# Performance work log

Measured on AMD Instinct MI355X. Metric: run time of the kernel, lower is better.

Reference implementation:

```python
import jax, jax.numpy as jnp
import numpy as np

B = 16
N = [20000, 5000, 1250, 313, 79]          # node counts per pooling level (fine -> coarse)
E = [120000, 30000, 7500, 1878, 474]      # ~6 edges per node (triangle mesh)
FILTERS = [3, 32, 32, 64, 64, 64]
K = 6
Z = 64
COND = 2
N_LAYERS = 4


def setup_inputs():
    ks = iter(jax.random.split(jax.random.key(0), 64))
    inp = {}
    inp["x"] = jax.random.normal(next(ks), (B * N[0], FILTERS[0]), jnp.float32)
    inp["label"] = jax.random.normal(next(ks), (B, COND), jnp.float32)
    for i in range(5):
        inp[f"edges{i}"] = jax.random.randint(next(ks), (2, E[i]), 0, N[i])
    for i in range(4):
        inp[f"ds_idx{i}"] = jax.random.randint(next(ks), (N[i + 1],), 0, N[i])
        inp[f"us_idx{i}"] = jax.random.randint(next(ks), (N[i], 3), 0, N[i + 1])
        inp[f"us_w{i}"] = jax.random.uniform(next(ks), (N[i], 3), jnp.float32)
    for i in range(4):
        inp[f"enc_w{i}"] = 0.1 * jax.random.normal(next(ks), (K, FILTERS[i], FILTERS[i + 1]), jnp.float32)
        inp[f"enc_b{i}"] = 0.1 * jax.random.normal(next(ks), (FILTERS[i + 1],), jnp.float32)
    for i in range(5):
        inp[f"dec_w{i}"] = 0.1 * jax.random.normal(next(ks), (K, FILTERS[-i - 1], FILTERS[-i - 2]), jnp.float32)
    for i in range(4):
        inp[f"dec_b{i}"] = 0.1 * jax.random.normal(next(ks), (FILTERS[-i - 2],), jnp.float32)
    lat_in = N[4] * FILTERS[-1]
    inp["enc_mu_w"] = 0.1 * jax.random.normal(next(ks), (lat_in, Z), jnp.float32)
    inp["enc_mu_b"] = jnp.zeros((Z,), jnp.float32)
    inp["enc_lv_w"] = 0.1 * jax.random.normal(next(ks), (lat_in, Z), jnp.float32)
    inp["enc_lv_b"] = jnp.zeros((Z,), jnp.float32)
    inp["dec_lin_w"] = 0.1 * jax.random.normal(next(ks), (Z + COND, lat_in), jnp.float32)
    inp["dec_lin_b"] = jnp.zeros((lat_in,), jnp.float32)
    return inp


def _sym_norm(edges, n):
    # ChebConv_Coma.norm: norm = D^-1/2[row] * w * D^-1/2[col], unit weights
    row, col = edges[0], edges[1]
    deg = jnp.zeros((n,), jnp.float32).at[row].add(1.0)
    dinv = jnp.where(deg > 0, deg ** -0.5, 0.0)
    return dinv[row] * dinv[col]


def _cheb(x, edges, norm, W, b):
    # Chebyshev recursion: Tx_0=x, Tx_1=L~x, Tx_k=2 L~ Tx_{k-1} - Tx_{k-2}
    src, tgt = edges[0], edges[1]

    def prop(h):  # h: [B, Nn, F] -> scatter-sum of norm-weighted source features
        return jnp.zeros_like(h).at[:, tgt].add(h[:, src] * norm[None, :, None])

    Tx0 = x
    out = jnp.einsum('bnf,fg->bng', Tx0, W[0])
    Tx1 = prop(x)
    out = out + jnp.einsum('bnf,fg->bng', Tx1, W[1])
    for k in range(2, W.shape[0]):
        Tx2 = 2.0 * prop(Tx1) - Tx0
        out = out + jnp.einsum('bnf,fg->bng', Tx2, W[k])
        Tx0, Tx1 = Tx1, Tx2
    return out if b is None else out + b


def _forward(x, label, us_ws, enc_ws, enc_bs, dec_ws, dec_bs,
             enc_mu_w, enc_mu_b, enc_lv_w, enc_lv_b, dec_lin_w, dec_lin_b,
             edges, norms, ds_idx, us_idx):
    h = x.reshape(B, N[0], FILTERS[0])
    # encoder
    for i in range(N_LAYERS):
        h = jax.nn.relu(_cheb(h, edges[i], norms[i], enc_ws[i], enc_bs[i]))
        h = h[:, ds_idx[i]]  # binary downsample matrix == row gather
    h = h.reshape(B, N[4] * FILTERS[-1])
    mu = h @ enc_mu_w + enc_mu_b
    logvar = h @ enc_lv_w + enc_lv_b
    # reparameterize (fixed eps for determinism)
    eps = jax.random.normal(jax.random.key(42), mu.shape, mu.dtype)
    z = mu + eps * jnp.exp(0.5 * logvar)
    # decoder
    h = jnp.concatenate([z, label], axis=1)
    h = jax.nn.relu(h @ dec_lin_w + dec_lin_b).reshape(B, N[4], FILTERS[-1])
    for i in range(N_LAYERS):
        lvl = N_LAYERS - 1 - i
        # barycentric upsample: 3 nonzeros per output row
        h = jnp.einsum('rk,brkf->brf', us_ws[lvl], h[:, us_idx[lvl]])
        h = jax.nn.relu(_cheb(h, edges[lvl], norms[lvl], dec_ws[i], dec_bs[i]))
    # faithful quirk of the original: final conv uses A_edge_index[-1] (coarsest graph edges)
    h = _cheb(h, edges[-1], norms[-1], dec_ws[4], None)
    return h.reshape(-1, FILTERS[0]), mu, logvar


def reference(x, label,
              edges0, edges1, edges2, edges3, edges4,
              ds_idx0, ds_idx1, ds_idx2, ds_idx3,
              us_idx0, us_idx1, us_idx2, us_idx3,
              us_w0, us_w1, us_w2, us_w3,
              enc_w0, enc_w1, enc_w2, enc_w3,
              enc_b0, enc_b1, enc_b2, enc_b3,
              dec_w0, dec_w1, dec_w2, dec_w3, dec_w4,
              dec_b0, dec_b1, dec_b2, dec_b3,
              enc_mu_w, enc_mu_b, enc_lv_w, enc_lv_b, dec_lin_w, dec_lin_b):
    edges = [edges0, edges1, edges2, edges3, edges4]
    norms = [_sym_norm(edges[i], N[i]) for i in range(5)]
    return _forward(x, label,
                    [us_w0, us_w1, us_w2, us_w3],
                    [enc_w0, enc_w1, enc_w2, enc_w3],
                    [enc_b0, enc_b1, enc_b2, enc_b3],
                    [dec_w0, dec_w1, dec_w2, dec_w3, dec_w4],
                    [dec_b0, dec_b1, dec_b2, dec_b3],
                    enc_mu_w, enc_mu_b, enc_lv_w, enc_lv_b, dec_lin_w, dec_lin_b,
                    edges, norms,
                    [ds_idx0, ds_idx1, ds_idx2, ds_idx3],
                    [us_idx0, us_idx1, us_idx2, us_idx3])
```

## Files before the change

### kernel.cpp

```cpp
#include <hip/hip_runtime.h>
#include <cstdint>
#include <cstddef>

#define WG 256
#define NB 16



__global__ void k_zero_i(int* __restrict__ p, int n) {
  int i = blockIdx.x * WG + threadIdx.x;
  if (i < n) p[i] = 0;
}

__global__ void k_hist(const int* __restrict__ edges, int E,
                       int* __restrict__ dsrc, int* __restrict__ dtgt) {
  int e = blockIdx.x * WG + threadIdx.x;
  if (e >= E) return;
  atomicAdd(&dsrc[edges[e]], 1);
  atomicAdd(&dtgt[edges[E + e]], 1);
}

__global__ void k_scan(const int* __restrict__ deg, int N,
                       int* __restrict__ rowptr, int* __restrict__ cursor) {
  __shared__ int s[WG];
  int t = threadIdx.x;
  int chunk = (N + WG - 1) / WG;
  int a = t * chunk;
  int b = min(N, a + chunk);
  int sum = 0;
  for (int i = a; i < b; i++) sum += deg[i];
  s[t] = sum;
  __syncthreads();
  for (int off = 1; off < WG; off <<= 1) {
    int v = (t >= off) ? s[t - off] : 0;
    __syncthreads();
    s[t] += v;
    __syncthreads();
  }
  int run = (t == 0) ? 0 : s[t - 1];
  for (int i = a; i < b; i++) {
    rowptr[i] = run;
    cursor[i] = run;
    run += deg[i];
  }
  if (t == 0) rowptr[N] = s[WG - 1];
}

__global__ void k_fill(const int* __restrict__ edges, int E,
                       const int* __restrict__ dsrc, int* __restrict__ cursor,
                       int* __restrict__ csrc, float* __restrict__ csw) {
  int e = blockIdx.x * WG + threadIdx.x;
  if (e >= E) return;
  int s = edges[e], t = edges[E + e];
  float da = (float)dsrc[s], db = (float)dsrc[t];
  float wa = (da > 0.f) ? (1.0f / sqrtf(da)) : 0.f;
  float wb = (db > 0.f) ? (1.0f / sqrtf(db)) : 0.f;
  int pos = atomicAdd(&cursor[t], 1);
  csrc[pos] = s;
  csw[pos] = wa * wb;
}

__global__ void k_tr_x(const float* __restrict__ x, float* __restrict__ out) {
  int i = blockIdx.x * WG + threadIdx.x;
  if (i >= NB * 20000 * 3) return;
  int f = i % 3;
  int b = (i / 3) % NB;
  int n = i / 48;
  out[i] = x[((size_t)b * 20000 + n) * 3 + f];
}


static __device__ __forceinline__ float erfinv_f(float x) {
  float w = -log1pf(-x * x);
  float p;
  if (w < 5.0f) {
    w -= 2.5f;
    p = 2.81022636e-08f;
    p = fmaf(p, w, 3.43273939e-07f);
    p = fmaf(p, w, -3.5233877e-06f);
    p = fmaf(p, w, -4.39150654e-06f);
    p = fmaf(p, w, 0.00021858087f);
    p = fmaf(p, w, -0.00125372503f);
    p = fmaf(p, w, -0.00417768164f);
    p = fmaf(p, w, 0.246640727f);
    p = fmaf(p, w, 1.50140941f);
  } else {
    w = sqrtf(w) - 3.0f;
    p = -0.000200214257f;
    p = fmaf(p, w, 0.000100950558f);
    p = fmaf(p, w, 0.00134934322f);
    p = fmaf(p, w, -0.00367342844f);
    p = fmaf(p, w, 0.00573950773f);
    p = fmaf(p, w, -0.0076224613f);
    p = fmaf(p, w, 0.00943887047f);
    p = fmaf(p, w, 1.00167406f);
    p = fmaf(p, w, 2.83297682f);
  }
  return p * x;
}

static __device__ __forceinline__ float bits_to_normal(unsigned b) {
  float f = __uint_as_float((b >> 9) | 0x3f800000u) - 1.0f;
  const float lo = -0.99999994f;
  float u = f * (1.0f - lo) + lo;
  u = fmaxf(u, lo);
  return 1.41421356f * erfinv_f(u);
}

__global__ void k_eps(float* __restrict__ eps) {
  int i = blockIdx.x * WG + threadIdx.x;
  if (i >= 1024) return;
  unsigned x0 = 0u, x1 = (unsigned)i;
  unsigned ks[3] = {0u, 42u, 0u ^ 42u ^ 0x1BD11BDAu};
  x0 += ks[0];
  x1 += ks[1];
  const int R[2][4] = {{13, 15, 26, 6}, {17, 29, 16, 24}};
#pragma unroll
  for (int it = 0; it < 5; it++) {
#pragma unroll
    for (int j = 0; j < 4; j++) {
      x0 += x1;
      int r = R[it & 1][j];
      x1 = (x1 << r) | (x1 >> (32 - r));
      x1 ^= x0;
    }
    x0 += ks[(it + 1) % 3];
    x1 += ks[(it + 2) % 3] + (unsigned)(it + 1);
  }
  eps[i] = bits_to_normal(x0 ^ x1);
}


template <int F>
__global__ __launch_bounds__(WG) void k_propw(const float* __restrict__ in,
                                              float* __restrict__ out,
                                              const float* __restrict__ sub, float scale,
                                              const int* __restrict__ rowptr,
                                              const int* __restrict__ csrc,
                                              const float* __restrict__ csw, int N) {
  constexpr int C4 = F / 16;
  int node = blockIdx.x * 4 + (threadIdx.x >> 6);
  if (node >= N) return;
  int lane = threadIdx.x & 63;
  const float4* in4 = (const float4*)in;
  float4 acc[C4];
#pragma unroll
  for (int u = 0; u < C4; u++) acc[u] = make_float4(0.f, 0.f, 0.f, 0.f);
  int beg = rowptr[node], end = rowptr[node + 1];
  int j = beg;
  for (; j + 1 < end; j += 2) {
    int s0 = __builtin_amdgcn_readfirstlane(csrc[j]);
    int s1 = __builtin_amdgcn_readfirstlane(csrc[j + 1]);
    float w0 = __int_as_float(__builtin_amdgcn_readfirstlane(__float_as_int(csw[j])));
    float w1 = __int_as_float(__builtin_amdgcn_readfirstlane(__float_as_int(csw[j + 1])));
    const float4* r0 = in4 + (size_t)s0 * (4 * F) + lane;
    const float4* r1 = in4 + (size_t)s1 * (4 * F) + lane;
#pragma unroll
    for (int u = 0; u < C4; u++) {
      float4 v0 = r0[u * 64];
      float4 v1 = r1[u * 64];
      acc[u].x = fmaf(w0, v0.x, acc[u].x); acc[u].y = fmaf(w0, v0.y, acc[u].y);
      acc[u].z = fmaf(w0, v0.z, acc[u].z); acc[u].w = fmaf(w0, v0.w, acc[u].w);
      acc[u].x = fmaf(w1, v1.x, acc[u].x); acc[u].y = fmaf(w1, v1.y, acc[u].y);
      acc[u].z = fmaf(w1, v1.z, acc[u].z); acc[u].w = fmaf(w1, v1.w, acc[u].w);
    }
  }
  if (j < end) {
    int s0 = __builtin_amdgcn_readfirstlane(csrc[j]);
    float w0 = __int_as_float(__builtin_amdgcn_readfirstlane(__float_as_int(csw[j])));
    const float4* r0 = in4 + (size_t)s0 * (4 * F) + lane;
#pragma unroll
    for (int u = 0; u < C4; u++) {
      float4 v0 = r0[u * 64];
      acc[u].x = fmaf(w0, v0.x, acc[u].x); acc[u].y = fmaf(w0, v0.y, acc[u].y);
      acc[u].z = fmaf(w0, v0.z, acc[u].z); acc[u].w = fmaf(w0, v0.w, acc[u].w);
    }
  }
  float4* o4 = (float4*)out + (size_t)node * (4 * F) + lane;
  if (sub) {
    const float4* s4 = (const float4*)sub + (size_t)node * (4 * F) + lane;
#pragma unroll
    for (int u = 0; u < C4; u++) {
      float4 sv = s4[u * 64];
      float4 r;
      r.x = fmaf(scale, acc[u].x, -sv.x); r.y = fmaf(scale, acc[u].y, -sv.y);
      r.z = fmaf(scale, acc[u].z, -sv.z); r.w = fmaf(scale, acc[u].w, -sv.w);
      o4[u * 64] = r;
    }
  } else {
#pragma unroll
    for (int u = 0; u < C4; u++) {
      float4 r;
      r.x = scale * acc[u].x; r.y = scale * acc[u].y;
      r.z = scale * acc[u].z; r.w = scale * acc[u].w;
      o4[u * 64] = r;
    }
  }
}

__global__ __launch_bounds__(WG) void k_propw3(const float* __restrict__ in,
                                               float* __restrict__ out,
                                               const float* __restrict__ sub, float scale,
                                               const int* __restrict__ rowptr,
                                               const int* __restrict__ csrc,
                                               const float* __restrict__ csw, int N) {
  int node = blockIdx.x * 4 + (threadIdx.x >> 6);
  if (node >= N) return;
  int lane = threadIdx.x & 63;
  if (lane >= 48) return;
  float acc = 0.f;
  int beg = rowptr[node], end = rowptr[node + 1];
  for (int j = beg; j < end; j++) {
    int s = __builtin_amdgcn_readfirstlane(csrc[j]);
    float w = __int_as_float(__builtin_amdgcn_readfirstlane(__float_as_int(csw[j])));
    acc = fmaf(w, in[(size_t)s * 48 + lane], acc);
  }
  float r = scale * acc;
  if (sub) r -= sub[(size_t)node * 48 + lane];
  out[(size_t)node * 48 + lane] = r;
}

struct Ptr3 {
  const float* p[3];
};

template <int F, int G>
__global__ __launch_bounds__(WG) void k_gemm3(Ptr3 txs, const float* __restrict__ W,
                                              const float* __restrict__ bias,
                                              float* __restrict__ out, int rows,
                                              const int* __restrict__ idx,
                                              int accum, int relu) {
  constexpr int CG = G / 4;
  constexpr int RT = WG / CG;
  constexpr int RPB = RT * 4;
  __shared__ float sW[3 * F * G];
  for (int i = threadIdx.x; i < 3 * F * G; i += WG) sW[i] = W[i];
  __syncthreads();
  int cg = threadIdx.x % CG;
  int rt = threadIdx.x / CG;
  int row0 = blockIdx.x * RPB + rt * 4;
  if (row0 >= rows) return;
  size_t src0;
  if (idx) {
    int node = row0 >> 4, b = row0 & 15;
    src0 = (size_t)idx[node] * 16 + b;
  } else {
    src0 = (size_t)row0;
  }
  float* o = out + (size_t)row0 * G + cg * 4;
  float4 acc[4];
  if (accum) {
#pragma unroll
    for (int r = 0; r < 4; r++) acc[r] = *(const float4*)(o + (size_t)r * G);
  } else if (bias) {
    float4 bv = *(const float4*)(bias + cg * 4);
#pragma unroll
    for (int r = 0; r < 4; r++) acc[r] = bv;
  } else {
#pragma unroll
    for (int r = 0; r < 4; r++) acc[r] = make_float4(0.f, 0.f, 0.f, 0.f);
  }
#pragma unroll
  for (int kk = 0; kk < 3; kk++) {
    const float* tb = txs.p[kk] + src0 * F;
    const float* w = sW + kk * F * G + cg * 4;
    if constexpr (F == 3) {
      float4 w0 = *(const float4*)(w + 0 * G);
      float4 w1 = *(const float4*)(w + 1 * G);
      float4 w2 = *(const float4*)(w + 2 * G);
#pragma unroll
      for (int r = 0; r < 4; r++) {
        float x0 = tb[r * 3 + 0], x1 = tb[r * 3 + 1], x2 = tb[r * 3 + 2];
        acc[r].x = fmaf(x0, w0.x, acc[r].x); acc[r].y = fmaf(x0, w0.y, acc[r].y);
        acc[r].z = fmaf(x0, w0.z, acc[r].z); acc[r].w = fmaf(x0, w0.w, acc[r].w);
        acc[r].x = fmaf(x1, w1.x, acc[r].x); acc[r].y = fmaf(x1, w1.y, acc[r].y);
        acc[r].z = fmaf(x1, w1.z, acc[r].z); acc[r].w = fmaf(x1, w1.w, acc[r].w);
        acc[r].x = fmaf(x2, w2.x, acc[r].x); acc[r].y = fmaf(x2, w2.y, acc[r].y);
        acc[r].z = fmaf(x2, w2.z, acc[r].z); acc[r].w = fmaf(x2, w2.w, acc[r].w);
      }
    } else {
#pragma unroll
      for (int fg = 0; fg < F / 4; fg++) {
        float4 w0 = *(const float4*)(w + (4 * fg + 0) * G);
        float4 w1 = *(const float4*)(w + (4 * fg + 1) * G);
        float4 w2 = *(const float4*)(w + (4 * fg + 2) * G);
        float4 w3 = *(const float4*)(w + (4 * fg + 3) * G);
#pragma unroll
        for (int r = 0; r < 4; r++) {
          float4 xv = *(const float4*)(tb + (size_t)r * F + 4 * fg);
          acc[r].x = fmaf(xv.x, w0.x, acc[r].x); acc[r].y = fmaf(xv.x, w0.y, acc[r].y);
          acc[r].z = fmaf(xv.x, w0.z, acc[r].z); acc[r].w = fmaf(xv.x, w0.w, acc[r].w);
          acc[r].x = fmaf(xv.y, w1.x, acc[r].x); acc[r].y = fmaf(xv.y, w1.y, acc[r].y);
          acc[r].z = fmaf(xv.y, w1.z, acc[r].z); acc[r].w = fmaf(xv.y, w1.w, acc[r].w);
          acc[r].x = fmaf(xv.z, w2.x, acc[r].x); acc[r].y = fmaf(xv.z, w2.y, acc[r].y);
          acc[r].z = fmaf(xv.z, w2.z, acc[r].z); acc[r].w = fmaf(xv.z, w2.w, acc[r].w);
          acc[r].x = fmaf(xv.w, w3.x, acc[r].x); acc[r].y = fmaf(xv.w, w3.y, acc[r].y);
          acc[r].z = fmaf(xv.w, w3.z, acc[r].z); acc[r].w = fmaf(xv.w, w3.w, acc[r].w);
        }
      }
    }
  }
  if (relu) {
#pragma unroll
    for (int r = 0; r < 4; r++) {
      acc[r].x = fmaxf(acc[r].x, 0.f); acc[r].y = fmaxf(acc[r].y, 0.f);
      acc[r].z = fmaxf(acc[r].z, 0.f); acc[r].w = fmaxf(acc[r].w, 0.f);
    }
  }
#pragma unroll
  for (int r = 0; r < 4; r++) *(float4*)(o + (size_t)r * G) = acc[r];
}

__global__ __launch_bounds__(WG) void k_final_short(const float* __restrict__ in,
                                                    const float* __restrict__ W,
                                                    float* __restrict__ out) {
  __shared__ float sW[96];
  if (threadIdx.x < 96)
    sW[threadIdx.x] = W[threadIdx.x] - W[192 + threadIdx.x] + W[384 + threadIdx.x];
  __syncthreads();
  int tid = blockIdx.x * WG + threadIdx.x;
  if (tid >= NB * 20000) return;
  int b = tid / 20000, n = tid % 20000;
  const float* t = in + ((size_t)n * 16 + b) * 32;
  float a0 = 0.f, a1 = 0.f, a2 = 0.f;
#pragma unroll
  for (int f = 0; f < 32; f += 4) {
    float4 v = *(const float4*)(t + f);
    a0 = fmaf(v.x, sW[(f + 0) * 3 + 0], a0); a1 = fmaf(v.x, sW[(f + 0) * 3 + 1], a1); a2 = fmaf(v.x, sW[(f + 0) * 3 + 2], a2);
    a0 = fmaf(v.y, sW[(f + 1) * 3 + 0], a0); a1 = fmaf(v.y, sW[(f + 1) * 3 + 1], a1); a2 = fmaf(v.y, sW[(f + 1) * 3 + 2], a2);
    a0 = fmaf(v.z, sW[(f + 2) * 3 + 0], a0); a1 = fmaf(v.z, sW[(f + 2) * 3 + 1], a1); a2 = fmaf(v.z, sW[(f + 2) * 3 + 2], a2);
    a0 = fmaf(v.w, sW[(f + 3) * 3 + 0], a0); a1 = fmaf(v.w, sW[(f + 3) * 3 + 1], a1); a2 = fmaf(v.w, sW[(f + 3) * 3 + 2], a2);
  }
  float* o = out + (size_t)tid * 3;
  o[0] = a0; o[1] = a1; o[2] = a2;
}

__global__ __launch_bounds__(256) void k_final_fix(const float* __restrict__ in,
                                                   const float* __restrict__ W,
                                                   const int* __restrict__ rowptr,
                                                   const int* __restrict__ csrc,
                                                   const float* __restrict__ csw,
                                                   float* __restrict__ out) {
  __shared__ float B0[79 * 32], B1[79 * 32], B2[79 * 32];
  __shared__ float sacc[79 * 3];
  __shared__ float sW[576];
  int b = blockIdx.x, t = threadIdx.x;
  for (int i = t; i < 576; i += 256) sW[i] = W[i];
  for (int i = t; i < 2528; i += 256) {
    int r = i >> 5, f = i & 31;
    B0[i] = in[((size_t)r * 16 + b) * 32 + f];
  }
  __syncthreads();
  for (int i = t; i < 237; i += 256) {
    int r = i / 3, g = i % 3;
    float a = 0.f;
    for (int f = 0; f < 32; f++) a = fmaf(B0[r * 32 + f], sW[f * 3 + g], a);
    sacc[i] = a;
  }
  for (int i = t; i < 2528; i += 256) {
    int r = i >> 5, f = i & 31;
    float a = 0.f;
    for (int j = rowptr[r]; j < rowptr[r + 1]; j++) a = fmaf(csw[j], B0[csrc[j] * 32 + f], a);
    B1[i] = a;
  }
  __syncthreads();
  for (int i = t; i < 237; i += 256) {
    int r = i / 3, g = i % 3;
    float a = sacc[i];
    for (int f = 0; f < 32; f++) a = fmaf(B1[r * 32 + f], sW[96 + f * 3 + g], a);
    sacc[i] = a;
  }
  for (int i = t; i < 2528; i += 256) {
    int r = i >> 5, f = i & 31;
    float a = 0.f;
    for (int j = rowptr[r]; j < rowptr[r + 1]; j++) a = fmaf(csw[j], B1[csrc[j] * 32 + f], a);
    B2[i] = 2.f * a - B0[i];
  }
  __syncthreads();
  for (int i = t; i < 237; i += 256) {
    int r = i / 3, g = i % 3;
    float a = sacc[i];
    for (int f = 0; f < 32; f++) a = fmaf(B2[r * 32 + f], sW[192 + f * 3 + g], a);
    sacc[i] = a;
  }
  __syncthreads();
  for (int i = t; i < 2528; i += 256) {
    int r = i >> 5, f = i & 31;
    float a = 0.f;
    for (int j = rowptr[r]; j < rowptr[r + 1]; j++) a = fmaf(csw[j], B2[csrc[j] * 32 + f], a);
    B0[i] = 2.f * a - B1[i];
  }
  __syncthreads();
  for (int i = t; i < 237; i += 256) {
    int r = i / 3, g = i % 3;
    float a = sacc[i];
    for (int f = 0; f < 32; f++) a = fmaf(B0[r * 32 + f], sW[288 + f * 3 + g], a);
    sacc[i] = a;
  }
  __syncthreads();
  for (int i = t; i < 2528; i += 256) {
    int r = i >> 5, f = i & 31;
    float a = 0.f;
    for (int j = rowptr[r]; j < rowptr[r + 1]; j++) a = fmaf(csw[j], B0[csrc[j] * 32 + f], a);
    B1[i] = 2.f * a - B2[i];
  }
  __syncthreads();
  for (int i = t; i < 237; i += 256) {
    int r = i / 3, g = i % 3;
    float a = sacc[i];
    for (int f = 0; f < 32; f++) a = fmaf(B1[r * 32 + f], sW[384 + f * 3 + g], a);
    sacc[i] = a;
  }
  __syncthreads();
  for (int i = t; i < 2528; i += 256) {
    int r = i >> 5, f = i & 31;
    float a = 0.f;
    for (int j = rowptr[r]; j < rowptr[r + 1]; j++) a = fmaf(csw[j], B1[csrc[j] * 32 + f], a);
    B2[i] = 2.f * a - B0[i];
  }
  __syncthreads();
  for (int i = t; i < 237; i += 256) {
    int r = i / 3, g = i % 3;
    float a = sacc[i];
    for (int f = 0; f < 32; f++) a = fmaf(B2[r * 32 + f], sW[480 + f * 3 + g], a);
    out[((size_t)b * 20000 + r) * 3 + g] = a;
  }
}

template <int F>
__global__ __launch_bounds__(WG) void k_us(const float* __restrict__ in,
                                           float* __restrict__ out,
                                           const int* __restrict__ uidx,
                                           const float* __restrict__ uw, int Nf) {
  int i = blockIdx.x * WG + threadIdx.x;
  int total = Nf * NB * F;
  if (i >= total) return;
  int pos = i % (NB * F);
  int r = i / (NB * F);
  float acc = 0.f;
#pragma unroll
  for (int k = 0; k < 3; k++) {
    float v = in[(size_t)uidx[r * 3 + k] * NB * F + pos];
    acc = fmaf(uw[r * 3 + k], fmaxf(v, 0.f), acc);
  }
  out[i] = acc;
}


__global__ __launch_bounds__(64) void k_latent(const float* __restrict__ h,
                                               const float* __restrict__ muW,
                                               const float* __restrict__ muB,
                                               const float* __restrict__ lvW,
                                               const float* __restrict__ lvB,
                                               const float* __restrict__ eps,
                                               const float* __restrict__ label,
                                               float* __restrict__ mu_out,
                                               float* __restrict__ lv_out,
                                               float* __restrict__ hcat) {
  int b = blockIdx.x / 64;
  int g = blockIdx.x % 64;
  int l = threadIdx.x;
  float am = 0.f, al = 0.f;
  for (int i = l; i < 5056; i += 64) {
    int n = i >> 6, f = i & 63;
    float hv = h[(size_t)(n * 16 + b) * 64 + f];
    am = fmaf(hv, muW[(size_t)i * 64 + g], am);
    al = fmaf(hv, lvW[(size_t)i * 64 + g], al);
  }
  for (int off = 32; off > 0; off >>= 1) {
    am += __shfl_down(am, off, 64);
    al += __shfl_down(al, off, 64);
  }
  if (l == 0) {
    am += muB[g];
    al += lvB[g];
    mu_out[b * 64 + g] = am;
    lv_out[b * 64 + g] = al;
    hcat[b * 66 + g] = fmaf(eps[b * 64 + g], expf(0.5f * al), am);
    if (g < 2) hcat[b * 66 + 64 + g] = label[b * 2 + g];
  }
}

__global__ __launch_bounds__(WG) void k_declin(const float* __restrict__ hcat,
                                               const float* __restrict__ W,
                                               const float* __restrict__ bias,
                                               float* __restrict__ out) {
  int idx = blockIdx.x * WG + threadIdx.x;
  if (idx >= NB * 5056) return;
  int b = idx / 5056, j = idx % 5056;
  int n = j >> 6, f = j & 63;
  float acc = bias[j];
  const float* hc = hcat + b * 66;
#pragma unroll
  for (int i = 0; i < 66; i++) acc = fmaf(hc[i], W[(size_t)i * 5056 + j], acc);
  out[(size_t)(n * 16 + b) * 64 + f] = fmaxf(acc, 0.f);
}


static inline dim3 grid1(long n) { return dim3((unsigned)((n + WG - 1) / WG)); }

template <int F, int G>
static void run_cheb(float* in, float* out, float* A, float* B,
                     const float* W, const float* bias, int N, int Nout,
                     const int* ds_idx, int relu_last,
                     const int* rowptr, const int* csrc, const float* csw,
                     hipStream_t st) {
  int orows = NB * Nout;
  constexpr int RPB = (WG / (G / 4)) * 4;
  dim3 gG((unsigned)((orows + RPB - 1) / RPB));
  dim3 gP((unsigned)((N + 3) / 4));
  int relu2 = ds_idx ? 1 : relu_last;
  if constexpr (F == 3) {
    k_propw3<<<gP, WG, 0, st>>>(in, A, nullptr, 1.f, rowptr, csrc, csw, N);
    k_propw3<<<gP, WG, 0, st>>>(A, B, in, 2.f, rowptr, csrc, csw, N);
    Ptr3 p1{{in, A, B}};
    k_gemm3<F, G><<<gG, WG, 0, st>>>(p1, W, bias, out, orows, ds_idx, 0, 0);
    k_propw3<<<gP, WG, 0, st>>>(B, in, A, 2.f, rowptr, csrc, csw, N);
    k_propw3<<<gP, WG, 0, st>>>(in, A, B, 2.f, rowptr, csrc, csw, N);
    k_propw3<<<gP, WG, 0, st>>>(A, B, in, 2.f, rowptr, csrc, csw, N);
    Ptr3 p2{{in, A, B}};
    k_gemm3<F, G><<<gG, WG, 0, st>>>(p2, W + 3 * F * G, nullptr, out, orows, ds_idx, 1, relu2);
  } else {
    k_propw<F><<<gP, WG, 0, st>>>(in, A, nullptr, 1.f, rowptr, csrc, csw, N);
    k_propw<F><<<gP, WG, 0, st>>>(A, B, in, 2.f, rowptr, csrc, csw, N);
    Ptr3 p1{{in, A, B}};
    k_gemm3<F, G><<<gG, WG, 0, st>>>(p1, W, bias, out, orows, ds_idx, 0, 0);
    k_propw<F><<<gP, WG, 0, st>>>(B, in, A, 2.f, rowptr, csrc, csw, N);
    k_propw<F><<<gP, WG, 0, st>>>(in, A, B, 2.f, rowptr, csrc, csw, N);
    k_propw<F><<<gP, WG, 0, st>>>(A, B, in, 2.f, rowptr, csrc, csw, N);
    Ptr3 p2{{in, A, B}};
    k_gemm3<F, G><<<gG, WG, 0, st>>>(p2, W + 3 * F * G, nullptr, out, orows, ds_idx, 1, relu2);
  }
}

extern "C" void kernel_launch(void* const* d_in, const int* in_sizes, int n_in,
                              void* d_out, int out_size, void* d_ws, size_t ws_size,
                              hipStream_t stream) {
  static const int NN[5] = {20000, 5000, 1250, 313, 79};
  static const int EE[5] = {120000, 30000, 7500, 1878, 474};
  static const int NCSR[5] = {20000, 5000, 1250, 313, 20000};

  const float* x = (const float*)d_in[0];
  const float* label = (const float*)d_in[1];
  const int* edges[5];
  for (int l = 0; l < 5; l++) edges[l] = (const int*)d_in[2 + l];
  const int* ds_idx[4];
  const int* us_idx[4];
  const float* us_w[4];
  for (int i = 0; i < 4; i++) {
    ds_idx[i] = (const int*)d_in[7 + 3 * i];
    us_idx[i] = (const int*)d_in[8 + 3 * i];
    us_w[i] = (const float*)d_in[9 + 3 * i];
  }
  const float* enc_w[4];
  const float* enc_b[4];
  for (int i = 0; i < 4; i++) {
    enc_w[i] = (const float*)d_in[19 + 2 * i];
    enc_b[i] = (const float*)d_in[20 + 2 * i];
  }
  const float* dec_w[5];
  for (int i = 0; i < 5; i++) dec_w[i] = (const float*)d_in[27 + i];
  const float* dec_b[4];
  for (int i = 0; i < 4; i++) dec_b[i] = (const float*)d_in[32 + i];
  const float* mu_w = (const float*)d_in[36];
  const float* mu_b = (const float*)d_in[37];
  const float* lv_w = (const float*)d_in[38];
  const float* lv_b = (const float*)d_in[39];
  const float* dl_w = (const float*)d_in[40];
  const float* dl_b = (const float*)d_in[41];

  float* wsf = (float*)d_ws;
  size_t off = 0;
  auto carve = [&](size_t n) -> float* {
    float* p = wsf + off;
    off += (n + 63) & ~(size_t)63;
    return p;
  };
  const size_t SLOT = 10240000;
  float* s0 = carve(SLOT);
  float* s1 = carve(SLOT);
  float* s2 = carve(SLOT);
  float* s3 = carve(SLOT);
  float* sxl = carve(960000);
  int* deg_all = (int*)carve(26642 + 46563);
  int* deg_src_all = deg_all;
  int* deg_tgt_all = deg_all + 26642;
  int* rowptr_all = (int*)carve(46568);
  int* cursor_all = (int*)carve(46563);
  int* csrc_all = (int*)carve(159852);
  float* csw_all = carve(159852);
  float* eps = carve(1024);
  float* hcat = carve(1056);

  int NOFF[5], COFF[5], ROFF[5], EOFF[5];
  {
    int na = 0, ca = 0, ra = 0, ea = 0;
    for (int l = 0; l < 5; l++) {
      NOFF[l] = na; na += NN[l];
      COFF[l] = ca; ca += NCSR[l];
      ROFF[l] = ra; ra += NCSR[l] + 1;
      EOFF[l] = ea; ea += EE[l];
    }
  }

  k_zero_i<<<grid1(26642 + 46563), WG, 0, stream>>>(deg_all, 26642 + 46563);
  for (int l = 0; l < 5; l++)
    k_hist<<<grid1(EE[l]), WG, 0, stream>>>(edges[l], EE[l], deg_src_all + NOFF[l],
                                            deg_tgt_all + COFF[l]);
  for (int l = 0; l < 5; l++)
    k_scan<<<1, WG, 0, stream>>>(deg_tgt_all + COFF[l], NCSR[l], rowptr_all + ROFF[l],
                                 cursor_all + COFF[l]);
  for (int l = 0; l < 5; l++)
    k_fill<<<grid1(EE[l]), WG, 0, stream>>>(edges[l], EE[l], deg_src_all + NOFF[l],
                                            cursor_all + COFF[l], csrc_all + EOFF[l],
                                            csw_all + EOFF[l]);
  k_eps<<<4, WG, 0, stream>>>(eps);
  k_tr_x<<<grid1(960000), WG, 0, stream>>>(x, sxl);

  auto RP = [&](int l) { return rowptr_all + ROFF[l]; };
  auto CS = [&](int l) { return csrc_all + EOFF[l]; };
  auto CW = [&](int l) { return csw_all + EOFF[l]; };

  float* mu_out = (float*)d_out + 960000;
  float* lv_out = (float*)d_out + 961024;

  run_cheb<3, 32>(sxl, s1, s2, s3, enc_w[0], enc_b[0], 20000, 5000, ds_idx[0], 0,
                  RP(0), CS(0), CW(0), stream);
  run_cheb<32, 32>(s1, s0, s2, s3, enc_w[1], enc_b[1], 5000, 1250, ds_idx[1], 0,
                   RP(1), CS(1), CW(1), stream);
  run_cheb<32, 64>(s0, s1, s2, s3, enc_w[2], enc_b[2], 1250, 313, ds_idx[2], 0,
                   RP(2), CS(2), CW(2), stream);
  run_cheb<64, 64>(s1, s0, s2, s3, enc_w[3], enc_b[3], 313, 79, ds_idx[3], 0,
                   RP(3), CS(3), CW(3), stream);

  k_latent<<<1024, 64, 0, stream>>>(s0, mu_w, mu_b, lv_w, lv_b, eps, label, mu_out, lv_out, hcat);
  k_declin<<<grid1(NB * 5056), WG, 0, stream>>>(hcat, dl_w, dl_b, s0);

  k_us<64><<<grid1((long)313 * NB * 64), WG, 0, stream>>>(s0, s1, us_idx[3], us_w[3], 313);
  run_cheb<64, 64>(s1, s0, s2, s3, dec_w[0], dec_b[0], 313, 313, nullptr, 0,
                   RP(3), CS(3), CW(3), stream);
  k_us<64><<<grid1((long)1250 * NB * 64), WG, 0, stream>>>(s0, s1, us_idx[2], us_w[2], 1250);
  run_cheb<64, 64>(s1, s0, s2, s3, dec_w[1], dec_b[1], 1250, 1250, nullptr, 0,
                   RP(2), CS(2), CW(2), stream);
  k_us<64><<<grid1((long)5000 * NB * 64), WG, 0, stream>>>(s0, s1, us_idx[1], us_w[1], 5000);
  run_cheb<64, 32>(s1, s0, s2, s3, dec_w[2], dec_b[2], 5000, 5000, nullptr, 0,
                   RP(1), CS(1), CW(1), stream);
  k_us<32><<<grid1((long)20000 * NB * 32), WG, 0, stream>>>(s0, s1, us_idx[0], us_w[0], 20000);
  run_cheb<32, 32>(s1, s0, s2, s3, dec_w[3], dec_b[3], 20000, 20000, nullptr, 1,
                   RP(0), CS(0), CW(0), stream);

  k_final_short<<<grid1(NB * 20000), WG, 0, stream>>>(s0, dec_w[4], (float*)d_out);
  k_final_fix<<<16, 256, 0, stream>>>(s0, dec_w[4], RP(4), CS(4), CW(4), (float*)d_out);
}
```

Before: 1.325 ms.

## Batch graph preprocessing launches, raise GEMM row tile, fuse final projection into GEMM

The per-level histogram, scan and CSR-fill launches are merged into single launches over all levels, and eps generation plus input transpose are folded into the fill kernel. The k_gemm3 row count per thread becomes a template parameter (8 for G=32), with input vectors loaded ahead of the FMAs. The last decoder Chebyshev GEMM is fused with the short final projection, which uses shuffle reductions and stores to s0 only for the first 79 nodes needed by the fix-up kernel. This cuts launch count and one full read of the 20000-node activations, at the cost of hardcoded sizes and more registers per thread.

```diff
diff --git a/kernel.cpp b/kernel.cpp
--- a/kernel.cpp
+++ b/kernel.cpp
@@ -6,23 +6,41 @@
 #define NB 16
 
 
+struct IP5 { const int* e[5]; };
+struct Ptr3 { const float* p[3]; };
+
 
 __global__ void k_zero_i(int* __restrict__ p, int n) {
   int i = blockIdx.x * WG + threadIdx.x;
   if (i < n) p[i] = 0;
 }
 
-__global__ void k_hist(const int* __restrict__ edges, int E,
-                       int* __restrict__ dsrc, int* __restrict__ dtgt) {
-  int e = blockIdx.x * WG + threadIdx.x;
-  if (e >= E) return;
-  atomicAdd(&dsrc[edges[e]], 1);
-  atomicAdd(&dtgt[edges[E + e]], 1);
-}
-
-__global__ void k_scan(const int* __restrict__ deg, int N,
-                       int* __restrict__ rowptr, int* __restrict__ cursor) {
+__global__ void k_hist_all(IP5 ep, int* __restrict__ dsrc, int* __restrict__ dtgt) {
+  int i = blockIdx.x * WG + threadIdx.x;
+  if (i >= 159852) return;
+  int l, eo, ee, no, co;
+  if (i < 120000)      { l = 0; eo = 0;      ee = 120000; no = 0;     co = 0; }
+  else if (i < 150000) { l = 1; eo = 120000; ee = 30000;  no = 20000; co = 20000; }
+  else if (i < 157500) { l = 2; eo = 150000; ee = 7500;   no = 25000; co = 25000; }
+  else if (i < 159378) { l = 3; eo = 157500; ee = 1878;   no = 26250; co = 26250; }
+  else                 { l = 4; eo = 159378; ee = 474;    no = 26563; co = 26563; }
+  int e = i - eo;
+  const int* E = ep.e[l];
+  atomicAdd(&dsrc[no + E[e]], 1);
+  atomicAdd(&dtgt[co + E[ee + e]], 1);
+}
+
+__global__ void k_scan_all(const int* __restrict__ deg_all, int* __restrict__ rowptr_all,
+                           int* __restrict__ cursor_all) {
+  static const int Ns[5] = {20000, 5000, 1250, 313, 20000};
+  static const int CO[5] = {0, 20000, 25000, 26250, 26563};
+  static const int RO[5] = {0, 20001, 25002, 26253, 26567};
   __shared__ int s[WG];
+  int l = blockIdx.x;
+  int N = Ns[l];
+  const int* deg = deg_all + CO[l];
+  int* rowptr = rowptr_all + RO[l];
+  int* cursor = cursor_all + CO[l];
   int t = threadIdx.x;
   int chunk = (N + WG - 1) / WG;
   int a = t * chunk;
@@ -44,29 +62,6 @@
     run += deg[i];
   }
   if (t == 0) rowptr[N] = s[WG - 1];
-}
-
-__global__ void k_fill(const int* __restrict__ edges, int E,
-                       const int* __restrict__ dsrc, int* __restrict__ cursor,
-                       int* __restrict__ csrc, float* __restrict__ csw) {
-  int e = blockIdx.x * WG + threadIdx.x;
-  if (e >= E) return;
-  int s = edges[e], t = edges[E + e];
-  float da = (float)dsrc[s], db = (float)dsrc[t];
-  float wa = (da > 0.f) ? (1.0f / sqrtf(da)) : 0.f;
-  float wb = (db > 0.f) ? (1.0f / sqrtf(db)) : 0.f;
-  int pos = atomicAdd(&cursor[t], 1);
-  csrc[pos] = s;
-  csw[pos] = wa * wb;
-}
-
-__global__ void k_tr_x(const float* __restrict__ x, float* __restrict__ out) {
-  int i = blockIdx.x * WG + threadIdx.x;
-  if (i >= NB * 20000 * 3) return;
-  int f = i % 3;
-  int b = (i / 3) % NB;
-  int n = i / 48;
-  out[i] = x[((size_t)b * 20000 + n) * 3 + f];
 }
 
 
@@ -107,9 +102,7 @@
   return 1.41421356f * erfinv_f(u);
 }
 
-__global__ void k_eps(float* __restrict__ eps) {
-  int i = blockIdx.x * WG + threadIdx.x;
-  if (i >= 1024) return;
+static __device__ __forceinline__ float eps_val(int i) {
   unsigned x0 = 0u, x1 = (unsigned)i;
   unsigned ks[3] = {0u, 42u, 0u ^ 42u ^ 0x1BD11BDAu};
   x0 += ks[0];
@@ -127,7 +120,43 @@
     x0 += ks[(it + 1) % 3];
     x1 += ks[(it + 2) % 3] + (unsigned)(it + 1);
   }
-  eps[i] = bits_to_normal(x0 ^ x1);
+  return bits_to_normal(x0 ^ x1);
+}
+
+__global__ void k_fill_all(IP5 ep, const int* __restrict__ dsrc, int* __restrict__ cursor,
+                           int* __restrict__ csrc, float* __restrict__ csw,
+                           float* __restrict__ eps, const float* __restrict__ x,
+                           float* __restrict__ sxl) {
+  int blk = blockIdx.x;
+  if (blk < 625) {
+    int i = blk * WG + threadIdx.x;
+    if (i >= 159852) return;
+    int l, eo, ee, no, co, eb;
+    if (i < 120000)      { l = 0; eo = 0;      ee = 120000; no = 0;     co = 0;     eb = 0; }
+    else if (i < 150000) { l = 1; eo = 120000; ee = 30000;  no = 20000; co = 20000; eb = 120000; }
+    else if (i < 157500) { l = 2; eo = 150000; ee = 7500;   no = 25000; co = 25000; eb = 150000; }
+    else if (i < 159378) { l = 3; eo = 157500; ee = 1878;   no = 26250; co = 26250; eb = 157500; }
+    else                 { l = 4; eo = 159378; ee = 474;    no = 26563; co = 26563; eb = 159378; }
+    int e = i - eo;
+    const int* E = ep.e[l];
+    int s = E[e], t = E[ee + e];
+    float da = (float)dsrc[no + s], db = (float)dsrc[no + t];
+    float wa = (da > 0.f) ? (1.0f / sqrtf(da)) : 0.f;
+    float wb = (db > 0.f) ? (1.0f / sqrtf(db)) : 0.f;
+    int pos = atomicAdd(&cursor[co + t], 1);
+    csrc[eb + pos] = s;
+    csw[eb + pos] = wa * wb;
+  } else if (blk < 629) {
+    int j = (blk - 625) * WG + threadIdx.x;
+    if (j < 1024) eps[j] = eps_val(j);
+  } else {
+    int j = (blk - 629) * WG + threadIdx.x;
+    if (j >= NB * 20000 * 3) return;
+    int f = j % 3;
+    int b = (j / 3) % NB;
+    int n = j / 48;
+    sxl[j] = x[((size_t)b * 20000 + n) * 3 + f];
+  }
 }
 
 
@@ -220,11 +249,8 @@
   out[(size_t)node * 48 + lane] = r;
 }
 
-struct Ptr3 {
-  const float* p[3];
-};
-
-template <int F, int G>
+
+template <int F, int G, int R>
 __global__ __launch_bounds__(WG) void k_gemm3(Ptr3 txs, const float* __restrict__ W,
                                               const float* __restrict__ bias,
                                               float* __restrict__ out, int rows,
@@ -232,33 +258,31 @@
                                               int accum, int relu) {
   constexpr int CG = G / 4;
   constexpr int RT = WG / CG;
-  constexpr int RPB = RT * 4;
+  constexpr int RPB = RT * R;
   __shared__ float sW[3 * F * G];
   for (int i = threadIdx.x; i < 3 * F * G; i += WG) sW[i] = W[i];
   __syncthreads();
   int cg = threadIdx.x % CG;
   int rt = threadIdx.x / CG;
-  int row0 = blockIdx.x * RPB + rt * 4;
+  int row0 = blockIdx.x * RPB + rt * R;
   if (row0 >= rows) return;
-  size_t src0;
+  size_t src0 = row0;
   if (idx) {
     int node = row0 >> 4, b = row0 & 15;
     src0 = (size_t)idx[node] * 16 + b;
-  } else {
-    src0 = (size_t)row0;
   }
   float* o = out + (size_t)row0 * G + cg * 4;
-  float4 acc[4];
+  float4 acc[R];
   if (accum) {
 #pragma unroll
-    for (int r = 0; r < 4; r++) acc[r] = *(const float4*)(o + (size_t)r * G);
+    for (int r = 0; r < R; r++) acc[r] = *(const float4*)(o + (size_t)r * G);
   } else if (bias) {
     float4 bv = *(const float4*)(bias + cg * 4);
 #pragma unroll
-    for (int r = 0; r < 4; r++) acc[r] = bv;
+    for (int r = 0; r < R; r++) acc[r] = bv;
   } else {
 #pragma unroll
-    for (int r = 0; r < 4; r++) acc[r] = make_float4(0.f, 0.f, 0.f, 0.f);
+    for (int r = 0; r < R; r++) acc[r] = make_float4(0.f, 0.f, 0.f, 0.f);
   }
 #pragma unroll
   for (int kk = 0; kk < 3; kk++) {
@@ -269,7 +293,7 @@
       float4 w1 = *(const float4*)(w + 1 * G);
       float4 w2 = *(const float4*)(w + 2 * G);
 #pragma unroll
-      for (int r = 0; r < 4; r++) {
+      for (int r = 0; r < R; r++) {
         float x0 = tb[r * 3 + 0], x1 = tb[r * 3 + 1], x2 = tb[r * 3 + 2];
         acc[r].x = fmaf(x0, w0.x, acc[r].x); acc[r].y = fmaf(x0, w0.y, acc[r].y);
         acc[r].z = fmaf(x0, w0.z, acc[r].z); acc[r].w = fmaf(x0, w0.w, acc[r].w);
@@ -281,58 +305,119 @@
     } else {
 #pragma unroll
       for (int fg = 0; fg < F / 4; fg++) {
+        float4 xv[R];
+#pragma unroll
+        for (int r = 0; r < R; r++) xv[r] = *(const float4*)(tb + (size_t)r * F + 4 * fg);
         float4 w0 = *(const float4*)(w + (4 * fg + 0) * G);
         float4 w1 = *(const float4*)(w + (4 * fg + 1) * G);
         float4 w2 = *(const float4*)(w + (4 * fg + 2) * G);
         float4 w3 = *(const float4*)(w + (4 * fg + 3) * G);
 #pragma unroll
-        for (int r = 0; r < 4; r++) {
-          float4 xv = *(const float4*)(tb + (size_t)r * F + 4 * fg);
-          acc[r].x = fmaf(xv.x, w0.x, acc[r].x); acc[r].y = fmaf(xv.x, w0.y, acc[r].y);
-          acc[r].z = fmaf(xv.x, w0.z, acc[r].z); acc[r].w = fmaf(xv.x, w0.w, acc[r].w);
-          acc[r].x = fmaf(xv.y, w1.x, acc[r].x); acc[r].y = fmaf(xv.y, w1.y, acc[r].y);
-          acc[r].z = fmaf(xv.y, w1.z, acc[r].z); acc[r].w = fmaf(xv.y, w1.w, acc[r].w);
-          acc[r].x = fmaf(xv.z, w2.x, acc[r].x); acc[r].y = fmaf(xv.z, w2.y, acc[r].y);
-          acc[r].z = fmaf(xv.z, w2.z, acc[r].z); acc[r].w = fmaf(xv.z, w2.w, acc[r].w);
-          acc[r].x = fmaf(xv.w, w3.x, acc[r].x); acc[r].y = fmaf(xv.w, w3.y, acc[r].y);
-          acc[r].z = fmaf(xv.w, w3.z, acc[r].z); acc[r].w = fmaf(xv.w, w3.w, acc[r].w);
+        for (int r = 0; r < R; r++) {
+          acc[r].x = fmaf(xv[r].x, w0.x, acc[r].x); acc[r].y = fmaf(xv[r].x, w0.y, acc[r].y);
+          acc[r].z = fmaf(xv[r].x, w0.z, acc[r].z); acc[r].w = fmaf(xv[r].x, w0.w, acc[r].w);
+          acc[r].x = fmaf(xv[r].y, w1.x, acc[r].x); acc[r].y = fmaf(xv[r].y, w1.y, acc[r].y);
+          acc[r].z = fmaf(xv[r].y, w1.z, acc[r].z); acc[r].w = fmaf(xv[r].y, w1.w, acc[r].w);
+          acc[r].x = fmaf(xv[r].z, w2.x, acc[r].x); acc[r].y = fmaf(xv[r].z, w2.y, acc[r].y);
+          acc[r].z = fmaf(xv[r].z, w2.z, acc[r].z); acc[r].w = fmaf(xv[r].z, w2.w, acc[r].w);
+          acc[r].x = fmaf(xv[r].w, w3.x, acc[r].x); acc[r].y = fmaf(xv[r].w, w3.y, acc[r].y);
+          acc[r].z = fmaf(xv[r].w, w3.z, acc[r].z); acc[r].w = fmaf(xv[r].w, w3.w, acc[r].w);
         }
       }
     }
   }
   if (relu) {
 #pragma unroll
-    for (int r = 0; r < 4; r++) {
+    for (int r = 0; r < R; r++) {
       acc[r].x = fmaxf(acc[r].x, 0.f); acc[r].y = fmaxf(acc[r].y, 0.f);
       acc[r].z = fmaxf(acc[r].z, 0.f); acc[r].w = fmaxf(acc[r].w, 0.f);
     }
   }
 #pragma unroll
-  for (int r = 0; r < 4; r++) *(float4*)(o + (size_t)r * G) = acc[r];
-}
-
-__global__ __launch_bounds__(WG) void k_final_short(const float* __restrict__ in,
-                                                    const float* __restrict__ W,
-                                                    float* __restrict__ out) {
-  __shared__ float sW[96];
+  for (int r = 0; r < R; r++) *(float4*)(o + (size_t)r * G) = acc[r];
+}
+
+__global__ __launch_bounds__(WG) void k_gemm3_final(Ptr3 txs, const float* __restrict__ W,
+                                                    const float* __restrict__ W4,
+                                                    float* __restrict__ out,
+                                                    float* __restrict__ dout, int rows) {
+  constexpr int F = 32, G = 32, R = 8;
+  constexpr int CG = G / 4;
+  constexpr int RT = WG / CG;
+  constexpr int RPB = RT * R;
+  __shared__ float sW[3 * F * G];
+  __shared__ float sWc[96];
+  for (int i = threadIdx.x; i < 3 * F * G; i += WG) sW[i] = W[i];
   if (threadIdx.x < 96)
-    sW[threadIdx.x] = W[threadIdx.x] - W[192 + threadIdx.x] + W[384 + threadIdx.x];
-  __syncthreads();
-  int tid = blockIdx.x * WG + threadIdx.x;
-  if (tid >= NB * 20000) return;
-  int b = tid / 20000, n = tid % 20000;
-  const float* t = in + ((size_t)n * 16 + b) * 32;
-  float a0 = 0.f, a1 = 0.f, a2 = 0.f;
-#pragma unroll
-  for (int f = 0; f < 32; f += 4) {
-    float4 v = *(const float4*)(t + f);
-    a0 = fmaf(v.x, sW[(f + 0) * 3 + 0], a0); a1 = fmaf(v.x, sW[(f + 0) * 3 + 1], a1); a2 = fmaf(v.x, sW[(f + 0) * 3 + 2], a2);
-    a0 = fmaf(v.y, sW[(f + 1) * 3 + 0], a0); a1 = fmaf(v.y, sW[(f + 1) * 3 + 1], a1); a2 = fmaf(v.y, sW[(f + 1) * 3 + 2], a2);
-    a0 = fmaf(v.z, sW[(f + 2) * 3 + 0], a0); a1 = fmaf(v.z, sW[(f + 2) * 3 + 1], a1); a2 = fmaf(v.z, sW[(f + 2) * 3 + 2], a2);
-    a0 = fmaf(v.w, sW[(f + 3) * 3 + 0], a0); a1 = fmaf(v.w, sW[(f + 3) * 3 + 1], a1); a2 = fmaf(v.w, sW[(f + 3) * 3 + 2], a2);
-  }
-  float* o = out + (size_t)tid * 3;
-  o[0] = a0; o[1] = a1; o[2] = a2;
+    sWc[threadIdx.x] = W4[threadIdx.x] - W4[192 + threadIdx.x] + W4[384 + threadIdx.x];
+  __syncthreads();
+  int cg = threadIdx.x % CG;
+  int rt = threadIdx.x / CG;
+  int row0 = blockIdx.x * RPB + rt * R;
+  float* o = out + (size_t)row0 * G + cg * 4;
+  float4 acc[R];
+#pragma unroll
+  for (int r = 0; r < R; r++) acc[r] = *(const float4*)(o + (size_t)r * G);
+#pragma unroll
+  for (int kk = 0; kk < 3; kk++) {
+    const float* tb = txs.p[kk] + (size_t)row0 * F;
+    const float* w = sW + kk * F * G + cg * 4;
+#pragma unroll
+    for (int fg = 0; fg < F / 4; fg++) {
+      float4 xv[R];
+#pragma unroll
+      for (int r = 0; r < R; r++) xv[r] = *(const float4*)(tb + (size_t)r * F + 4 * fg);
+      float4 w0 = *(const float4*)(w + (4 * fg + 0) * G);
+      float4 w1 = *(const float4*)(w + (4 * fg + 1) * G);
+      float4 w2 = *(const float4*)(w + (4 * fg + 2) * G);
+      float4 w3 = *(const float4*)(w + (4 * fg + 3) * G);
+#pragma unroll
+      for (int r = 0; r < R; r++) {
+        acc[r].x = fmaf(xv[r].x, w0.x, acc[r].x); acc[r].y = fmaf(xv[r].x, w0.y, acc[r].y);
+        acc[r].z = fmaf(xv[r].x, w0.z, acc[r].z); acc[r].w = fmaf(xv[r].x, w0.w, acc[r].w);
+        acc[r].x = fmaf(xv[r].y, w1.x, acc[r].x); acc[r].y = fmaf(xv[r].y, w1.y, acc[r].y);
+        acc[r].z = fmaf(xv[r].y, w1.z, acc[r].z); acc[r].w = fmaf(xv[r].y, w1.w, acc[r].w);
+        acc[r].x = fmaf(xv[r].z, w2.x, acc[r].x); acc[r].y = fmaf(xv[r].z, w2.y, acc[r].y);
+        acc[r].z = fmaf(xv[r].z, w2.z, acc[r].z); acc[r].w = fmaf(xv[r].z, w2.w, acc[r].w);
+        acc[r].x = fmaf(xv[r].w, w3.x, acc[r].x); acc[r].y = fmaf(xv[r].w, w3.y, acc[r].y);
+        acc[r].z = fmaf(xv[r].w, w3.z, acc[r].z); acc[r].w = fmaf(xv[r].w, w3.w, acc[r].w);
+      }
+    }
+  }
+#pragma unroll
+  for (int r = 0; r < R; r++) {
+    acc[r].x = fmaxf(acc[r].x, 0.f); acc[r].y = fmaxf(acc[r].y, 0.f);
+    acc[r].z = fmaxf(acc[r].z, 0.f); acc[r].w = fmaxf(acc[r].w, 0.f);
+  }
+  int node0 = row0 >> 4;
+  if (node0 < 79) {
+#pragma unroll
+    for (int r = 0; r < R; r++) *(float4*)(o + (size_t)r * G) = acc[r];
+  }
+#pragma unroll
+  for (int r = 0; r < R; r++) {
+    float av[4] = {acc[r].x, acc[r].y, acc[r].z, acc[r].w};
+    float p0 = 0.f, p1 = 0.f, p2 = 0.f;
+#pragma unroll
+    for (int j = 0; j < 4; j++) {
+      int f = cg * 4 + j;
+      p0 = fmaf(av[j], sWc[f * 3 + 0], p0);
+      p1 = fmaf(av[j], sWc[f * 3 + 1], p1);
+      p2 = fmaf(av[j], sWc[f * 3 + 2], p2);
+    }
+#pragma unroll
+    for (int m = 4; m >= 1; m >>= 1) {
+      p0 += __shfl_xor(p0, m, 64);
+      p1 += __shfl_xor(p1, m, 64);
+      p2 += __shfl_xor(p2, m, 64);
+    }
+    if (cg == 0) {
+      int row = row0 + r;
+      int n = row >> 4, b = row & 15;
+      float* od = dout + ((size_t)b * 20000 + n) * 3;
+      od[0] = p0; od[1] = p1; od[2] = p2;
+    }
+  }
 }
 
 __global__ __launch_bounds__(256) void k_final_fix(const float* __restrict__ in,
@@ -506,7 +591,8 @@
                      const int* rowptr, const int* csrc, const float* csw,
                      hipStream_t st) {
   int orows = NB * Nout;
-  constexpr int RPB = (WG / (G / 4)) * 4;
+  constexpr int R = (G == 32) ? 8 : 4;
+  constexpr int RPB = (WG / (G / 4)) * R;
   dim3 gG((unsigned)((orows + RPB - 1) / RPB));
   dim3 gP((unsigned)((N + 3) / 4));
   int relu2 = ds_idx ? 1 : relu_last;
@@ -514,36 +600,32 @@
     k_propw3<<<gP, WG, 0, st>>>(in, A, nullptr, 1.f, rowptr, csrc, csw, N);
     k_propw3<<<gP, WG, 0, st>>>(A, B, in, 2.f, rowptr, csrc, csw, N);
     Ptr3 p1{{in, A, B}};
-    k_gemm3<F, G><<<gG, WG, 0, st>>>(p1, W, bias, out, orows, ds_idx, 0, 0);
+    k_gemm3<F, G, R><<<gG, WG, 0, st>>>(p1, W, bias, out, orows, ds_idx, 0, 0);
     k_propw3<<<gP, WG, 0, st>>>(B, in, A, 2.f, rowptr, csrc, csw, N);
     k_propw3<<<gP, WG, 0, st>>>(in, A, B, 2.f, rowptr, csrc, csw, N);
     k_propw3<<<gP, WG, 0, st>>>(A, B, in, 2.f, rowptr, csrc, csw, N);
     Ptr3 p2{{in, A, B}};
-    k_gemm3<F, G><<<gG, WG, 0, st>>>(p2, W + 3 * F * G, nullptr, out, orows, ds_idx, 1, relu2);
+    k_gemm3<F, G, R><<<gG, WG, 0, st>>>(p2, W + 3 * F * G, nullptr, out, orows, ds_idx, 1, relu2);
   } else {
     k_propw<F><<<gP, WG, 0, st>>>(in, A, nullptr, 1.f, rowptr, csrc, csw, N);
     k_propw<F><<<gP, WG, 0, st>>>(A, B, in, 2.f, rowptr, csrc, csw, N);
     Ptr3 p1{{in, A, B}};
-    k_gemm3<F, G><<<gG, WG, 0, st>>>(p1, W, bias, out, orows, ds_idx, 0, 0);
+    k_gemm3<F, G, R><<<gG, WG, 0, st>>>(p1, W, bias, out, orows, ds_idx, 0, 0);
     k_propw<F><<<gP, WG, 0, st>>>(B, in, A, 2.f, rowptr, csrc, csw, N);
     k_propw<F><<<gP, WG, 0, st>>>(in, A, B, 2.f, rowptr, csrc, csw, N);
     k_propw<F><<<gP, WG, 0, st>>>(A, B, in, 2.f, rowptr, csrc, csw, N);
     Ptr3 p2{{in, A, B}};
-    k_gemm3<F, G><<<gG, WG, 0, st>>>(p2, W + 3 * F * G, nullptr, out, orows, ds_idx, 1, relu2);
+    k_gemm3<F, G, R><<<gG, WG, 0, st>>>(p2, W + 3 * F * G, nullptr, out, orows, ds_idx, 1, relu2);
   }
 }
 
 extern "C" void kernel_launch(void* const* d_in, const int* in_sizes, int n_in,
                               void* d_out, int out_size, void* d_ws, size_t ws_size,
                               hipStream_t stream) {
-  static const int NN[5] = {20000, 5000, 1250, 313, 79};
-  static const int EE[5] = {120000, 30000, 7500, 1878, 474};
-  static const int NCSR[5] = {20000, 5000, 1250, 313, 20000};
-
   const float* x = (const float*)d_in[0];
   const float* label = (const float*)d_in[1];
-  const int* edges[5];
-  for (int l = 0; l < 5; l++) edges[l] = (const int*)d_in[2 + l];
+  IP5 ep;
+  for (int l = 0; l < 5; l++) ep.e[l] = (const int*)d_in[2 + l];
   const int* ds_idx[4];
   const int* us_idx[4];
   const float* us_w[4];
@@ -592,34 +674,17 @@
   float* eps = carve(1024);
   float* hcat = carve(1056);
 
-  int NOFF[5], COFF[5], ROFF[5], EOFF[5];
-  {
-    int na = 0, ca = 0, ra = 0, ea = 0;
-    for (int l = 0; l < 5; l++) {
-      NOFF[l] = na; na += NN[l];
-      COFF[l] = ca; ca += NCSR[l];
-      ROFF[l] = ra; ra += NCSR[l] + 1;
-      EOFF[l] = ea; ea += EE[l];
-    }
-  }
-
-  k_zero_i<<<grid1(26642 + 46563), WG, 0, stream>>>(deg_all, 26642 + 46563);
-  for (int l = 0; l < 5; l++)
-    k_hist<<<grid1(EE[l]), WG, 0, stream>>>(edges[l], EE[l], deg_src_all + NOFF[l],
-                                            deg_tgt_all + COFF[l]);
-  for (int l = 0; l < 5; l++)
-    k_scan<<<1, WG, 0, stream>>>(deg_tgt_all + COFF[l], NCSR[l], rowptr_all + ROFF[l],
-                                 cursor_all + COFF[l]);
-  for (int l = 0; l < 5; l++)
-    k_fill<<<grid1(EE[l]), WG, 0, stream>>>(edges[l], EE[l], deg_src_all + NOFF[l],
-                                            cursor_all + COFF[l], csrc_all + EOFF[l],
-                                            csw_all + EOFF[l]);
-  k_eps<<<4, WG, 0, stream>>>(eps);
-  k_tr_x<<<grid1(960000), WG, 0, stream>>>(x, sxl);
-
+  static const int ROFF[5] = {0, 20001, 25002, 26253, 26567};
+  static const int EOFF[5] = {0, 120000, 150000, 157500, 159378};
   auto RP = [&](int l) { return rowptr_all + ROFF[l]; };
   auto CS = [&](int l) { return csrc_all + EOFF[l]; };
   auto CW = [&](int l) { return csw_all + EOFF[l]; };
+
+  k_zero_i<<<grid1(26642 + 46563), WG, 0, stream>>>(deg_all, 26642 + 46563);
+  k_hist_all<<<grid1(159852), WG, 0, stream>>>(ep, deg_src_all, deg_tgt_all);
+  k_scan_all<<<5, WG, 0, stream>>>(deg_tgt_all, rowptr_all, cursor_all);
+  k_fill_all<<<625 + 4 + 3750, WG, 0, stream>>>(ep, deg_src_all, cursor_all, csrc_all,
+                                                csw_all, eps, x, sxl);
 
   float* mu_out = (float*)d_out + 960000;
   float* lv_out = (float*)d_out + 961024;
@@ -646,9 +711,23 @@
   run_cheb<64, 32>(s1, s0, s2, s3, dec_w[2], dec_b[2], 5000, 5000, nullptr, 0,
                    RP(1), CS(1), CW(1), stream);
   k_us<32><<<grid1((long)20000 * NB * 32), WG, 0, stream>>>(s0, s1, us_idx[0], us_w[0], 20000);
-  run_cheb<32, 32>(s1, s0, s2, s3, dec_w[3], dec_b[3], 20000, 20000, nullptr, 1,
-                   RP(0), CS(0), CW(0), stream);
-
-  k_final_short<<<grid1(NB * 20000), WG, 0, stream>>>(s0, dec_w[4], (float*)d_out);
+
+  {
+    const int N = 20000;
+    int rows = NB * N;
+    dim3 gP((unsigned)((N + 3) / 4));
+    dim3 gG((unsigned)(rows / 256));
+    k_propw<32><<<gP, WG, 0, stream>>>(s1, s2, nullptr, 1.f, RP(0), CS(0), CW(0), N);
+    k_propw<32><<<gP, WG, 0, stream>>>(s2, s3, s1, 2.f, RP(0), CS(0), CW(0), N);
+    Ptr3 p1{{s1, s2, s3}};
+    k_gemm3<32, 32, 8><<<gG, WG, 0, stream>>>(p1, dec_w[3], dec_b[3], s0, rows, nullptr, 0, 0);
+    k_propw<32><<<gP, WG, 0, stream>>>(s3, s1, s2, 2.f, RP(0), CS(0), CW(0), N);
+    k_propw<32><<<gP, WG, 0, stream>>>(s1, s2, s3, 2.f, RP(0), CS(0), CW(0), N);
+    k_propw<32><<<gP, WG, 0, stream>>>(s2, s3, s1, 2.f, RP(0), CS(0), CW(0), N);
+    Ptr3 p2{{s1, s2, s3}};
+    k_gemm3_final<<<gG, WG, 0, stream>>>(p2, dec_w[3] + 3 * 32 * 32, dec_w[4], s0,
+                                         (float*)d_out, rows);
+  }
+
   k_final_fix<<<16, 256, 0, stream>>>(s0, dec_w[4], RP(4), CS(4), CW(4), (float*)d_out);
 }
```

Result: no change. 1.343 ms (+1.4%).
